# Kernel tuning notes

Measured on AMD Instinct MI355X. Metric: run time of the kernel, lower is better.

## Reference

```python
import jax, jax.numpy as jnp
import numpy as np
import math

B, L, E, H, G = 2, 128, 1024, 16, 8
D = E // H   # head_dim = 64
R = H // G   # query heads per kv head = 2


def setup_inputs() -> dict:
    key = jax.random.key(0)
    ks = jax.random.split(key, 12)
    def nrm(k, shape, s=1.0):
        return jax.random.normal(k, shape, dtype=jnp.float32) * s
    return {
        "Q": nrm(ks[0], (B, L, E)),
        "K": nrm(ks[1], (B, L, E)),
        "V": nrm(ks[2], (B, L, E)),
        "rpe": nrm(ks[3], (B, L, L, E)),
        "ln_g": jnp.ones((E,), jnp.float32),
        "ln_b": jnp.zeros((E,), jnp.float32),
        "Wq": nrm(ks[4], (E, H * D), 0.02), "bq": jnp.zeros((H * D,), jnp.float32),
        "Wk": nrm(ks[5], (E, G * D), 0.02), "bk": jnp.zeros((G * D,), jnp.float32),
        "Wv": nrm(ks[6], (E, G * D), 0.02), "bv": jnp.zeros((G * D,), jnp.float32),
        "Wrk": nrm(ks[7], (E, G * D), 0.02), "brk": jnp.zeros((G * D,), jnp.float32),
        "Wrv": nrm(ks[8], (E, G * D), 0.02), "brv": jnp.zeros((G * D,), jnp.float32),
        "Wo": nrm(ks[9], (E, E), 0.02), "bo": jnp.zeros((E,), jnp.float32),
    }


def _layernorm(x, g, b, eps=1e-5):
    mu = jnp.mean(x, axis=-1, keepdims=True)
    var = jnp.var(x, axis=-1, keepdims=True)
    return (x - mu) * jax.lax.rsqrt(var + eps) * g + b


def reference(Q, K, V, rpe, ln_g, ln_b, Wq, bq, Wk, bk, Wv, bv, Wrk, brk, Wrv, brv, Wo, bo):
    q = (Q @ Wq + bq).reshape(B, L, H, D).transpose(0, 2, 1, 3)   # [B,H,L,D]
    k = (K @ Wk + bk).reshape(B, L, G, D).transpose(0, 2, 1, 3)   # [B,G,L,D]
    v = (V @ Wv + bv).reshape(B, L, G, D).transpose(0, 2, 1, 3)   # [B,G,L,D]

    rn = _layernorm(rpe, ln_g, ln_b)                              # [B,L,L,E]
    rpe_k = (rn @ Wrk + brk).reshape(B, L, L, G, D).transpose(0, 3, 1, 2, 4)  # [B,G,L,L,D]
    rpe_v = (rn @ Wrv + brv).reshape(B, L, L, G, D).transpose(0, 3, 1, 2, 4)

    # Group query heads: head h = g*R + r maps to kv group g (repeat_interleave semantics).
    qg = q.reshape(B, G, R, L, D)
    # score[b,h,i,j] = q[b,h,i] . (k[b,g,i] + rpe_k[b,g,i,j]) / sqrt(D)
    # (note: the original pairs q_i with k_i, only rpe_k carries j-dependence)
    base = jnp.einsum('bgrid,bgid->bgri', qg, k)                  # j-independent q.k
    cross = jnp.einsum('bgrid,bgijd->bgrij', qg, rpe_k)
    scores = (base[..., None] + cross) / math.sqrt(D)             # [B,G,R,L,L]

    # Faithful to F.softmax over flattened L*L axis per head.
    attn = jax.nn.softmax(scores.reshape(B, G, R, L * L), axis=-1).reshape(B, G, R, L, L)

    # qv[b,h,i] = sum_j attn[b,h,i,j] * (v[b,g,i] + rpe_v[b,g,i,j])
    wsum = jnp.sum(attn, axis=-1)                                 # [B,G,R,L]
    qv = wsum[..., None] * v[:, :, None] + jnp.einsum('bgrij,bgijd->bgrid', attn, rpe_v)
    qv = qv.reshape(B, H, L, D).transpose(0, 2, 1, 3).reshape(B, L, E)
    return qv @ Wo + bo
```

## Files before the change

### kernel.cpp

```cpp
#include <hip/hip_runtime.h>


__global__ __launch_bounds__(256) void k_zero(
    const float* __restrict__ bq, const float* __restrict__ bk, const float* __restrict__ bv,
    const float* __restrict__ bo,
    float* __restrict__ q_ws, float* __restrict__ k_ws, float* __restrict__ v_ws,
    float* __restrict__ qv_ws, float* __restrict__ out, float* __restrict__ Gu_ws)
{
  int rr = blockIdx.x, tid = threadIdx.x;
#pragma unroll
  for (int s = 0; s < 4; s++) {
    int i = tid + s * 256;
    q_ws[rr * 1024 + i] = bq[i];
    qv_ws[rr * 1024 + i] = 0.f;
    out[rr * 1024 + i] = bo[i];
  }
#pragma unroll
  for (int s = 0; s < 2; s++) {
    int i = tid + s * 256;
    k_ws[rr * 512 + i] = bk[i];
    v_ws[rr * 512 + i] = bv[i];
  }
  int t = rr * 256 + tid;
  if (t < 4096) Gu_ws[t] = 0.f;
}

__global__ __launch_bounds__(256) void k_qkv(
    const float* __restrict__ Q, const float* __restrict__ K, const float* __restrict__ V,
    const float* __restrict__ Wq, const float* __restrict__ Wk, const float* __restrict__ Wv,
    float* __restrict__ q_ws, float* __restrict__ k_ws, float* __restrict__ v_ws)
{
  __shared__ float xs[8][256];
  int ct = blockIdx.x, rt = blockIdx.y, es = blockIdx.z, tid = threadIdx.x;
  const float* X; const float* W; float* out; int ldW, ldO, c0;
  if (ct < 4)      { X = Q; W = Wq; out = q_ws; ldW = 1024; ldO = 1024; c0 = ct * 256; }
  else if (ct < 6) { X = K; W = Wk; out = k_ws; ldW = 512;  ldO = 512;  c0 = (ct - 4) * 256; }
  else             { X = V; W = Wv; out = v_ws; ldW = 512;  ldO = 512;  c0 = (ct - 6) * 256; }
  int row0 = rt * 8, e0 = es * 256;
  for (int f = tid; f < 512; f += 256) {
    int r = f >> 6, e4 = f & 63;
    *(float4*)&xs[r][e4 * 4] = *(const float4*)(X + (size_t)(row0 + r) * 1024 + e0 + e4 * 4);
  }
  __syncthreads();
  int cg = tid & 63, rs = tid >> 6;
  int c = c0 + cg * 4;
  const float* wp = W + (size_t)e0 * ldW + c;
  float a0[4] = {0, 0, 0, 0}, a1[4] = {0, 0, 0, 0};
  float4 wc = *(const float4*)wp;
  for (int e = 0; e < 256; e++) {
    int en = e + 1 < 256 ? e + 1 : 255;
    float4 wn = *(const float4*)(wp + (size_t)en * ldW);
    float x0 = xs[rs][e], x1 = xs[rs + 4][e];
    a0[0] += x0 * wc.x; a0[1] += x0 * wc.y; a0[2] += x0 * wc.z; a0[3] += x0 * wc.w;
    a1[0] += x1 * wc.x; a1[1] += x1 * wc.y; a1[2] += x1 * wc.z; a1[3] += x1 * wc.w;
    wc = wn;
  }
#pragma unroll
  for (int s = 0; s < 4; s++) {
    atomicAdd(out + (size_t)(row0 + rs) * ldO + c + s, a0[s]);
    atomicAdd(out + (size_t)(row0 + rs + 4) * ldO + c + s, a1[s]);
  }
}

__global__ __launch_bounds__(256) void k_base(
    const float* __restrict__ q_ws, const float* __restrict__ k_ws,
    const float* __restrict__ brk, float* __restrict__ S0_ws)
{
  int t = blockIdx.x * 256 + threadIdx.x;
  int r = t >> 4, h = t & 15, g = h >> 1;
  const float* qp = q_ws + r * 1024 + h * 64;
  const float* kp = k_ws + r * 512 + g * 64;
  const float* bp = brk + g * 64;
  float s = 0.f;
#pragma unroll
  for (int d4 = 0; d4 < 16; d4++) {
    float4 q4 = *(const float4*)(qp + d4 * 4);
    float4 k4 = *(const float4*)(kp + d4 * 4);
    float4 b4 = *(const float4*)(bp + d4 * 4);
    s += q4.x * (k4.x + b4.x) + q4.y * (k4.y + b4.y)
       + q4.z * (k4.z + b4.z) + q4.w * (k4.w + b4.w);
  }
  S0_ws[t] = s * 0.125f;
}

__global__ __launch_bounds__(256) void k_uproj(
    const float* __restrict__ q_ws, const float* __restrict__ Wrk,
    const float* __restrict__ lng, const float* __restrict__ lnb,
    float* __restrict__ ut_ws, float* __restrict__ Gu_ws, float* __restrict__ S0_ws)
{
  __shared__ float wt[64][128];
  __shared__ float qs[32][64];
  int et = blockIdx.x, rrt = blockIdx.y, g = blockIdx.z, tid = threadIdx.x;
  int e0 = et * 128, rr0 = rrt * 16;
  for (int f = tid; f < 2048; f += 256) {
    int er = f >> 4, dq = f & 15;
    float4 p = *(const float4*)(Wrk + (size_t)(e0 + er) * 512 + g * 64 + dq * 4);
    wt[dq * 4 + 0][er] = p.x; wt[dq * 4 + 1][er] = p.y;
    wt[dq * 4 + 2][er] = p.z; wt[dq * 4 + 3][er] = p.w;
  }
  for (int f = tid; f < 512; f += 256) {
    int m = f >> 4, dq = f & 15;
    int rr = rr0 + (m >> 1), h = g * 2 + (m & 1);
    float4 p = *(const float4*)(q_ws + (size_t)rr * 1024 + h * 64 + dq * 4);
    qs[m][dq * 4 + 0] = p.x; qs[m][dq * 4 + 1] = p.y;
    qs[m][dq * 4 + 2] = p.z; qs[m][dq * 4 + 3] = p.w;
  }
  __syncthreads();
  int eg = tid & 31, rs = tid >> 5;
  float acc[4][4];
#pragma unroll
  for (int i = 0; i < 4; i++)
#pragma unroll
    for (int s = 0; s < 4; s++) acc[i][s] = 0.f;
  for (int d = 0; d < 64; d++) {
    float4 wv = *(float4*)&wt[d][eg * 4];
#pragma unroll
    for (int i = 0; i < 4; i++) {
      float qv = qs[rs * 4 + i][d];
      acc[i][0] += qv * wv.x; acc[i][1] += qv * wv.y;
      acc[i][2] += qv * wv.z; acc[i][3] += qv * wv.w;
    }
  }
#pragma unroll
  for (int k = 0; k < 2; k++) {
    int rr = rr0 + rs * 2 + k;
#pragma unroll
    for (int s = 0; s < 4; s++) {
      int e = e0 + eg * 4 + s;
      float2 st;
      st.x = acc[2 * k][s] * 0.125f;
      st.y = acc[2 * k + 1][s] * 0.125f;
      *(float2*)(ut_ws + ((size_t)rr * 1024 + e) * 16 + g * 2) = st;
    }
  }
  float4 ge4 = *(const float4*)(lng + e0 + eg * 4);
  float4 be4 = *(const float4*)(lnb + e0 + eg * 4);
#pragma unroll
  for (int i = 0; i < 4; i++) {
    float pg = 0.125f * (ge4.x * acc[i][0] + ge4.y * acc[i][1] + ge4.z * acc[i][2] + ge4.w * acc[i][3]);
    float pb = 0.125f * (be4.x * acc[i][0] + be4.y * acc[i][1] + be4.z * acc[i][2] + be4.w * acc[i][3]);
#pragma unroll
    for (int mk = 16; mk >= 1; mk >>= 1) { pg += __shfl_xor(pg, mk); pb += __shfl_xor(pb, mk); }
    if (eg == 0) {
      int m = rs * 4 + i;
      int rr = rr0 + (m >> 1), h = g * 2 + (m & 1);
      atomicAdd(Gu_ws + rr * 16 + h, pg);
      atomicAdd(S0_ws + rr * 16 + h, pb);
    }
  }
}

__global__ __launch_bounds__(128) void k_dotp(
    const float* __restrict__ rpe, const float* __restrict__ lng,
    const float* __restrict__ ut_ws, const float* __restrict__ Gu_ws,
    const float* __restrict__ S0_ws,
    float* __restrict__ s_ws, float* __restrict__ mu_ws, float* __restrict__ rs_ws)
{
  __shared__ float xs[32][68];
  __shared__ float us_t[16][68];
  int jt = blockIdx.x, rr = blockIdx.y, tid = threadIdx.x;
  int hq = tid & 7, jq = tid >> 3;
  int j0 = jt * 32;
  float acc[2][2] = {{0.f, 0.f}, {0.f, 0.f}};
  float sx[2] = {0.f, 0.f}, sq[2] = {0.f, 0.f};

  for (int ec = 0; ec < 16; ec++) {
    int eb = ec * 64;
    __syncthreads();
#pragma unroll
    for (int it = 0; it < 4; it++) {
      int f = it * 128 + tid;
      int row = f >> 4, e4 = f & 15;
      *(float4*)&xs[row][e4 * 4] =
          *(const float4*)(rpe + ((size_t)(rr * 128 + j0 + row)) * 1024 + eb + e4 * 4);
    }
#pragma unroll
    for (int it = 0; it < 2; it++) {
      int f = it * 128 + tid;
      int e = f >> 2, hh = f & 3;
      float4 u4 = *(const float4*)(ut_ws + ((size_t)rr * 1024 + eb + e) * 16 + hh * 4);
      float ge = lng[eb + e];
      us_t[hh * 4 + 0][e] = u4.x * ge;
      us_t[hh * 4 + 1][e] = u4.y * ge;
      us_t[hh * 4 + 2][e] = u4.z * ge;
      us_t[hh * 4 + 3][e] = u4.w * ge;
    }
    __syncthreads();
#pragma unroll
    for (int e4 = 0; e4 < 16; e4++) {
      float4 u0 = *(float4*)&us_t[hq * 2 + 0][e4 * 4];
      float4 u1 = *(float4*)&us_t[hq * 2 + 1][e4 * 4];
#pragma unroll
      for (int i = 0; i < 2; i++) {
        float4 xv = *(float4*)&xs[jq * 2 + i][e4 * 4];
        acc[i][0] += xv.x * u0.x + xv.y * u0.y + xv.z * u0.z + xv.w * u0.w;
        acc[i][1] += xv.x * u1.x + xv.y * u1.y + xv.z * u1.z + xv.w * u1.w;
        sx[i] += xv.x + xv.y + xv.z + xv.w;
        sq[i] += xv.x * xv.x + xv.y * xv.y + xv.z * xv.z + xv.w * xv.w;
      }
    }
  }
  float2 Gu2 = *(const float2*)(Gu_ws + rr * 16 + hq * 2);
  float2 S02 = *(const float2*)(S0_ws + rr * 16 + hq * 2);
#pragma unroll
  for (int i = 0; i < 2; i++) {
    int j = j0 + jq * 2 + i;
    float mu = sx[i] * (1.f / 1024.f);
    float rsv = rsqrtf(fmaxf(sq[i] * (1.f / 1024.f) - mu * mu, 0.f) + 1e-5f);
    float2 o;
    o.x = S02.x + rsv * (acc[i][0] - mu * Gu2.x);
    o.y = S02.y + rsv * (acc[i][1] - mu * Gu2.y);
    *(float2*)(s_ws + ((size_t)rr * 128 + j) * 16 + hq * 2) = o;
    if (hq == 0) { mu_ws[rr * 128 + j] = mu; rs_ws[rr * 128 + j] = rsv; }
  }
}

__global__ __launch_bounds__(256) void k_attn_p(
    const float* __restrict__ mu_ws, const float* __restrict__ rs_ws,
    float* __restrict__ s_ws,
    float* __restrict__ M_ws, float* __restrict__ Z_ws, float* __restrict__ C1_ws)
{
  int rr = blockIdx.x, tid = threadIdx.x;
  int h = tid >> 4, jl = tid & 15;
  float sv[8];
  float m = -1e30f;
#pragma unroll
  for (int k = 0; k < 8; k++) {
    int j = jl + k * 16;
    sv[k] = s_ws[((size_t)rr * 128 + j) * 16 + h];
    m = fmaxf(m, sv[k]);
  }
#pragma unroll
  for (int mk = 8; mk >= 1; mk >>= 1) m = fmaxf(m, __shfl_xor(m, mk, 16));
  float z = 0.f, c1 = 0.f;
#pragma unroll
  for (int k = 0; k < 8; k++) {
    int j = jl + k * 16;
    float p = expf(sv[k] - m);
    z += p;
    float p2 = p * rs_ws[rr * 128 + j];
    c1 += p2 * mu_ws[rr * 128 + j];
    s_ws[((size_t)rr * 128 + j) * 16 + h] = p2;
  }
#pragma unroll
  for (int mk = 8; mk >= 1; mk >>= 1) { z += __shfl_xor(z, mk, 16); c1 += __shfl_xor(c1, mk, 16); }
  if (jl == 0) {
    M_ws[rr * 16 + h] = m; Z_ws[rr * 16 + h] = z; C1_ws[rr * 16 + h] = c1;
  }
}

__global__ __launch_bounds__(128) void k_comb(
    const float* __restrict__ M_ws, const float* __restrict__ Z_ws, float* __restrict__ sc_ws)
{
  __shared__ float red[128];
  int b = blockIdx.x >> 4, h = blockIdx.x & 15;
  int i = threadIdx.x;
  int idx = ((b << 7) + i) * 16 + h;
  float ml = M_ws[idx];
  red[i] = ml;
  __syncthreads();
  for (int s = 64; s >= 1; s >>= 1) {
    if (i < s) red[i] = fmaxf(red[i], red[i + s]);
    __syncthreads();
  }
  float mg = red[0];
  __syncthreads();
  float zl = Z_ws[idx] * expf(ml - mg);
  red[i] = zl;
  __syncthreads();
  for (int s = 64; s >= 1; s >>= 1) {
    if (i < s) red[i] += red[i + s];
    __syncthreads();
  }
  float zg = red[0];
  sc_ws[idx] = expf(ml - mg) / zg;
}

__global__ __launch_bounds__(256) void k_wun(
    const float* __restrict__ rpe, const float* __restrict__ lng, const float* __restrict__ lnb,
    const float* __restrict__ p2_ws,
    const float* __restrict__ Z_ws, const float* __restrict__ C1_ws,
    float* __restrict__ w_ws)
{
  __shared__ float xs[16][512];
  __shared__ float p2s[128][16];
  __shared__ float C1S[16], ZS[16];
  int es = blockIdx.x, rr = blockIdx.y, tid = threadIdx.x;
  int e0 = es * 512;
#pragma unroll
  for (int it = 0; it < 2; it++) {
    int f = it * 256 + tid;
    int jj = f >> 2, hh = f & 3;
    *(float4*)&p2s[jj][hh * 4] = *(const float4*)(p2_ws + ((size_t)rr * 128 + jj) * 16 + hh * 4);
  }
  if (tid < 16) { C1S[tid] = C1_ws[rr * 16 + tid]; ZS[tid] = Z_ws[rr * 16 + tid]; }
  float acc[2][16];
#pragma unroll
  for (int i = 0; i < 2; i++)
#pragma unroll
    for (int h = 0; h < 16; h++) acc[i][h] = 0.f;

#define WUN_ROW(ii, xval) \
  acc[ii][0] += (xval) * p0.x;  acc[ii][1] += (xval) * p0.y;  \
  acc[ii][2] += (xval) * p0.z;  acc[ii][3] += (xval) * p0.w;  \
  acc[ii][4] += (xval) * p1.x;  acc[ii][5] += (xval) * p1.y;  \
  acc[ii][6] += (xval) * p1.z;  acc[ii][7] += (xval) * p1.w;  \
  acc[ii][8] += (xval) * p2v.x; acc[ii][9] += (xval) * p2v.y; \
  acc[ii][10] += (xval) * p2v.z; acc[ii][11] += (xval) * p2v.w; \
  acc[ii][12] += (xval) * p3.x; acc[ii][13] += (xval) * p3.y; \
  acc[ii][14] += (xval) * p3.z; acc[ii][15] += (xval) * p3.w;

  for (int jc = 0; jc < 8; jc++) {
    __syncthreads();
#pragma unroll
    for (int it = 0; it < 8; it++) {
      int f = it * 256 + tid;
      int row = f >> 7, e4 = f & 127;
      *(float4*)&xs[row][e4 * 4] =
          *(const float4*)(rpe + ((size_t)(rr * 128 + jc * 16 + row)) * 1024 + e0 + e4 * 4);
    }
    __syncthreads();
#pragma unroll
    for (int j = 0; j < 16; j++) {
      int jj = jc * 16 + j;
      float2 xv = *(float2*)&xs[j][tid * 2];
      float4 p0 = *(float4*)&p2s[jj][0];
      float4 p1 = *(float4*)&p2s[jj][4];
      float4 p2v = *(float4*)&p2s[jj][8];
      float4 p3 = *(float4*)&p2s[jj][12];
      WUN_ROW(0, xv.x)
      WUN_ROW(1, xv.y)
    }
  }
#undef WUN_ROW

#pragma unroll
  for (int i = 0; i < 2; i++) {
    int e = e0 + tid * 2 + i;
    float ge = lng[e], be = lnb[e];
    float* wp = w_ws + ((size_t)rr * 1024 + e) * 16;
#pragma unroll
    for (int hh = 0; hh < 4; hh++) {
      float4 o;
      o.x = ge * (acc[i][hh * 4 + 0] - C1S[hh * 4 + 0]) + be * ZS[hh * 4 + 0];
      o.y = ge * (acc[i][hh * 4 + 1] - C1S[hh * 4 + 1]) + be * ZS[hh * 4 + 1];
      o.z = ge * (acc[i][hh * 4 + 2] - C1S[hh * 4 + 2]) + be * ZS[hh * 4 + 2];
      o.w = ge * (acc[i][hh * 4 + 3] - C1S[hh * 4 + 3]) + be * ZS[hh * 4 + 3];
      *(float4*)(wp + hh * 4) = o;
    }
  }
}

__global__ __launch_bounds__(256) void k_qv(
    const float* __restrict__ w_ws, const float* __restrict__ Wrv,
    float* __restrict__ qv_ws)
{
  __shared__ float As[32][133];
  int g = blockIdx.x, rrt = blockIdx.y, es = blockIdx.z, tid = threadIdx.x;
  int rr0 = rrt * 16, e0 = es * 128;
  for (int f = tid; f < 2048; f += 256) {
    int rl = f >> 7, e = f & 127;
    float2 w2 = *(const float2*)(w_ws + ((size_t)(rr0 + rl) * 1024 + e0 + e) * 16 + g * 2);
    As[rl * 2 + 0][e] = w2.x;
    As[rl * 2 + 1][e] = w2.y;
  }
  __syncthreads();
  int cl = tid & 15, ms = tid >> 4;
  const float* wp = Wrv + (size_t)e0 * 512 + g * 64 + cl * 4;
  float acc[2][4];
#pragma unroll
  for (int hh = 0; hh < 2; hh++)
#pragma unroll
    for (int s = 0; s < 4; s++) acc[hh][s] = 0.f;
  float4 wc = *(const float4*)wp;
  for (int e = 0; e < 128; e++) {
    int en = e + 1 < 128 ? e + 1 : 127;
    float4 wn = *(const float4*)(wp + (size_t)en * 512);
    float a0 = As[ms * 2][e], a1 = As[ms * 2 + 1][e];
    acc[0][0] += a0 * wc.x; acc[0][1] += a0 * wc.y; acc[0][2] += a0 * wc.z; acc[0][3] += a0 * wc.w;
    acc[1][0] += a1 * wc.x; acc[1][1] += a1 * wc.y; acc[1][2] += a1 * wc.z; acc[1][3] += a1 * wc.w;
    wc = wn;
  }
  int rr = rr0 + ms;
#pragma unroll
  for (int hh = 0; hh < 2; hh++) {
    float* qp = qv_ws + (size_t)rr * 1024 + (g * 2 + hh) * 64 + cl * 4;
#pragma unroll
    for (int s = 0; s < 4; s++) atomicAdd(qp + s, acc[hh][s]);
  }
}

__global__ __launch_bounds__(256) void k_out(
    const float* __restrict__ qv_ws, const float* __restrict__ v_ws,
    const float* __restrict__ brv, const float* __restrict__ Z_ws,
    const float* __restrict__ sc_ws, const float* __restrict__ Wo,
    float* __restrict__ out)
{
  __shared__ float xs[8][128];
  int ct = blockIdx.x, rt = blockIdx.y, es = blockIdx.z, tid = threadIdx.x;
  int row0 = rt * 8, e0 = es * 128, c0 = ct * 256;
  for (int f = tid; f < 1024; f += 256) {
    int r = f >> 7, ei = f & 127;
    int e = e0 + ei, row = row0 + r;
    int h = e >> 6, gg = h >> 1, dl = e & 63;
    float vb = v_ws[row * 512 + gg * 64 + dl] + brv[gg * 64 + dl];
    xs[r][ei] = sc_ws[row * 16 + h] * (Z_ws[row * 16 + h] * vb + qv_ws[(size_t)row * 1024 + e]);
  }
  __syncthreads();
  int cg = tid & 63, rs = tid >> 6;
  int c = c0 + cg * 4;
  const float* wp = Wo + (size_t)e0 * 1024 + c;
  float a0[4] = {0, 0, 0, 0}, a1[4] = {0, 0, 0, 0};
  float4 wc = *(const float4*)wp;
  for (int e = 0; e < 128; e++) {
    int en = e + 1 < 128 ? e + 1 : 127;
    float4 wn = *(const float4*)(wp + (size_t)en * 1024);
    float x0 = xs[rs][e], x1 = xs[rs + 4][e];
    a0[0] += x0 * wc.x; a0[1] += x0 * wc.y; a0[2] += x0 * wc.z; a0[3] += x0 * wc.w;
    a1[0] += x1 * wc.x; a1[1] += x1 * wc.y; a1[2] += x1 * wc.z; a1[3] += x1 * wc.w;
    wc = wn;
  }
#pragma unroll
  for (int s = 0; s < 4; s++) {
    atomicAdd(out + (size_t)(row0 + rs) * 1024 + c + s, a0[s]);
    atomicAdd(out + (size_t)(row0 + rs + 4) * 1024 + c + s, a1[s]);
  }
}

extern "C" void kernel_launch(void* const* d_in, const int* in_sizes, int n_in,
                              void* d_out, int out_size, void* d_ws, size_t ws_size,
                              hipStream_t stream) {
  (void)in_sizes; (void)n_in; (void)out_size; (void)ws_size;
  const float* Q   = (const float*)d_in[0];
  const float* K   = (const float*)d_in[1];
  const float* V   = (const float*)d_in[2];
  const float* rpe = (const float*)d_in[3];
  const float* lng = (const float*)d_in[4];
  const float* lnb = (const float*)d_in[5];
  const float* Wq  = (const float*)d_in[6];
  const float* bq  = (const float*)d_in[7];
  const float* Wk  = (const float*)d_in[8];
  const float* bk  = (const float*)d_in[9];
  const float* Wv  = (const float*)d_in[10];
  const float* bv  = (const float*)d_in[11];
  const float* Wrk = (const float*)d_in[12];
  const float* brk = (const float*)d_in[13];
  const float* Wrv = (const float*)d_in[14];
  const float* brv = (const float*)d_in[15];
  const float* Wo  = (const float*)d_in[16];
  const float* bo  = (const float*)d_in[17];
  float* out = (float*)d_out;

  float* ws    = (float*)d_ws;
  float* q_ws  = ws;
  float* k_ws  = q_ws + 262144;
  float* v_ws  = k_ws + 131072;
  float* ut_ws = v_ws + 131072;
  float* S0_ws = ut_ws + 4194304;
  float* Gu_ws = S0_ws + 4096;
  float* s_ws  = Gu_ws + 4096;
  float* mu_ws = s_ws + 524288;
  float* rs_ws = mu_ws + 32768;
  float* M_ws  = rs_ws + 32768;
  float* Z_ws  = M_ws + 4096;
  float* C1_ws = Z_ws + 4096;
  float* sc_ws = C1_ws + 4096;
  float* qv_ws = sc_ws + 4096;
  float* w_ws  = ut_ws;

  k_zero<<<256, 256, 0, stream>>>(bq, bk, bv, bo, q_ws, k_ws, v_ws, qv_ws, out, Gu_ws);
  k_qkv<<<dim3(8, 32, 4), 256, 0, stream>>>(Q, K, V, Wq, Wk, Wv, q_ws, k_ws, v_ws);
  k_base<<<16, 256, 0, stream>>>(q_ws, k_ws, brk, S0_ws);
  k_uproj<<<dim3(8, 16, 8), 256, 0, stream>>>(q_ws, Wrk, lng, lnb, ut_ws, Gu_ws, S0_ws);
  k_dotp<<<dim3(4, 256), 128, 0, stream>>>(rpe, lng, ut_ws, Gu_ws, S0_ws, s_ws, mu_ws, rs_ws);
  k_attn_p<<<256, 256, 0, stream>>>(mu_ws, rs_ws, s_ws, M_ws, Z_ws, C1_ws);
  k_comb<<<32, 128, 0, stream>>>(M_ws, Z_ws, sc_ws);
  k_wun<<<dim3(2, 256), 256, 0, stream>>>(rpe, lng, lnb, s_ws, Z_ws, C1_ws, w_ws);
  k_qv<<<dim3(8, 16, 8), 256, 0, stream>>>(w_ws, Wrv, qv_ws);
  k_out<<<dim3(4, 32, 8), 256, 0, stream>>>(qv_ws, v_ws, brv, Z_ws, sc_ws, Wo, out);
}
```

Measured before the change: 506.8 us.

## Split k_dotp reduction over E into two halves and finalize in k_attn_p

The rpe dot-product kernel now splits the 1024-wide embedding reduction into two halves across a new grid dimension, doubling block count. Partial dot products and partial sum/sumsq statistics go to separate buffers, and the layernorm normalization and score assembly move into k_attn_p, which adds the two partials. Each thread now computes only part of the row sum/sumsq (a redundancy removal), followed by a shuffle reduction. This adds extra workspace traffic and requires the workspace to be large enough for the new buffers.

```diff
diff --git a/kernel.cpp b/kernel.cpp
--- a/kernel.cpp
+++ b/kernel.cpp
@@ -152,20 +152,22 @@
 
 __global__ __launch_bounds__(128) void k_dotp(
     const float* __restrict__ rpe, const float* __restrict__ lng,
-    const float* __restrict__ ut_ws, const float* __restrict__ Gu_ws,
-    const float* __restrict__ S0_ws,
-    float* __restrict__ s_ws, float* __restrict__ mu_ws, float* __restrict__ rs_ws)
+    const float* __restrict__ ut_ws,
+    float* __restrict__ sraw0, float* __restrict__ sraw1,
+    float* __restrict__ sxp0, float* __restrict__ sxp1,
+    float* __restrict__ sqp0, float* __restrict__ sqp1)
 {
   __shared__ float xs[32][68];
   __shared__ float us_t[16][68];
-  int jt = blockIdx.x, rr = blockIdx.y, tid = threadIdx.x;
+  int jt = blockIdx.x, rr = blockIdx.y, et = blockIdx.z, tid = threadIdx.x;
   int hq = tid & 7, jq = tid >> 3;
   int j0 = jt * 32;
+  int ebase = et * 512;
   float acc[2][2] = {{0.f, 0.f}, {0.f, 0.f}};
   float sx[2] = {0.f, 0.f}, sq[2] = {0.f, 0.f};
 
-  for (int ec = 0; ec < 16; ec++) {
-    int eb = ec * 64;
+  for (int ec = 0; ec < 8; ec++) {
+    int eb = ebase + ec * 64;
     __syncthreads();
 #pragma unroll
     for (int it = 0; it < 4; it++) {
@@ -195,39 +197,64 @@
         float4 xv = *(float4*)&xs[jq * 2 + i][e4 * 4];
         acc[i][0] += xv.x * u0.x + xv.y * u0.y + xv.z * u0.z + xv.w * u0.w;
         acc[i][1] += xv.x * u1.x + xv.y * u1.y + xv.z * u1.z + xv.w * u1.w;
+      }
+    }
+#pragma unroll
+    for (int t = 0; t < 2; t++) {
+      int e4s = t * 8 + hq;
+#pragma unroll
+      for (int i = 0; i < 2; i++) {
+        float4 xv = *(float4*)&xs[jq * 2 + i][e4s * 4];
         sx[i] += xv.x + xv.y + xv.z + xv.w;
         sq[i] += xv.x * xv.x + xv.y * xv.y + xv.z * xv.z + xv.w * xv.w;
       }
     }
   }
-  float2 Gu2 = *(const float2*)(Gu_ws + rr * 16 + hq * 2);
-  float2 S02 = *(const float2*)(S0_ws + rr * 16 + hq * 2);
+  float* sr = (et == 0) ? sraw0 : sraw1;
+  float* sxp = (et == 0) ? sxp0 : sxp1;
+  float* sqp = (et == 0) ? sqp0 : sqp1;
 #pragma unroll
   for (int i = 0; i < 2; i++) {
     int j = j0 + jq * 2 + i;
-    float mu = sx[i] * (1.f / 1024.f);
-    float rsv = rsqrtf(fmaxf(sq[i] * (1.f / 1024.f) - mu * mu, 0.f) + 1e-5f);
-    float2 o;
-    o.x = S02.x + rsv * (acc[i][0] - mu * Gu2.x);
-    o.y = S02.y + rsv * (acc[i][1] - mu * Gu2.y);
-    *(float2*)(s_ws + ((size_t)rr * 128 + j) * 16 + hq * 2) = o;
-    if (hq == 0) { mu_ws[rr * 128 + j] = mu; rs_ws[rr * 128 + j] = rsv; }
+    float2 o; o.x = acc[i][0]; o.y = acc[i][1];
+    *(float2*)(sr + ((size_t)rr * 128 + j) * 16 + hq * 2) = o;
+#pragma unroll
+    for (int mk = 4; mk >= 1; mk >>= 1) {
+      sx[i] += __shfl_xor(sx[i], mk, 8);
+      sq[i] += __shfl_xor(sq[i], mk, 8);
+    }
+    if (hq == 0) {
+      sxp[rr * 128 + j] = sx[i];
+      sqp[rr * 128 + j] = sq[i];
+    }
   }
 }
 
 __global__ __launch_bounds__(256) void k_attn_p(
-    const float* __restrict__ mu_ws, const float* __restrict__ rs_ws,
+    const float* __restrict__ sraw0, const float* __restrict__ sraw1,
+    const float* __restrict__ sxp0, const float* __restrict__ sxp1,
+    const float* __restrict__ sqp0, const float* __restrict__ sqp1,
+    const float* __restrict__ Gu_ws, const float* __restrict__ S0_ws,
     float* __restrict__ s_ws,
     float* __restrict__ M_ws, float* __restrict__ Z_ws, float* __restrict__ C1_ws)
 {
   int rr = blockIdx.x, tid = threadIdx.x;
   int h = tid >> 4, jl = tid & 15;
-  float sv[8];
+  float Gv = Gu_ws[rr * 16 + h];
+  float S0v = S0_ws[rr * 16 + h];
+  float sv[8], muv[8], rsvv[8];
   float m = -1e30f;
 #pragma unroll
   for (int k = 0; k < 8; k++) {
     int j = jl + k * 16;
-    sv[k] = s_ws[((size_t)rr * 128 + j) * 16 + h];
+    size_t idx = ((size_t)rr * 128 + j) * 16 + h;
+    float sxv = sxp0[rr * 128 + j] + sxp1[rr * 128 + j];
+    float sqv = sqp0[rr * 128 + j] + sqp1[rr * 128 + j];
+    float mu = sxv * (1.f / 1024.f);
+    float rsv = rsqrtf(fmaxf(sqv * (1.f / 1024.f) - mu * mu, 0.f) + 1e-5f);
+    float accv = sraw0[idx] + sraw1[idx];
+    sv[k] = S0v + rsv * (accv - mu * Gv);
+    muv[k] = mu; rsvv[k] = rsv;
     m = fmaxf(m, sv[k]);
   }
 #pragma unroll
@@ -238,8 +265,8 @@
     int j = jl + k * 16;
     float p = expf(sv[k] - m);
     z += p;
-    float p2 = p * rs_ws[rr * 128 + j];
-    c1 += p2 * mu_ws[rr * 128 + j];
+    float p2 = p * rsvv[k];
+    c1 += p2 * muv[k];
     s_ws[((size_t)rr * 128 + j) * 16 + h] = p2;
   }
 #pragma unroll
@@ -466,14 +493,22 @@
   float* C1_ws = Z_ws + 4096;
   float* sc_ws = C1_ws + 4096;
   float* qv_ws = sc_ws + 4096;
+  float* sraw0 = qv_ws + 262144;
+  float* sraw1 = sraw0 + 524288;
+  float* sxp0  = sraw1 + 524288;
+  float* sxp1  = sxp0 + 32768;
+  float* sqp0  = sxp1 + 32768;
+  float* sqp1  = sqp0 + 32768;
   float* w_ws  = ut_ws;
 
   k_zero<<<256, 256, 0, stream>>>(bq, bk, bv, bo, q_ws, k_ws, v_ws, qv_ws, out, Gu_ws);
   k_qkv<<<dim3(8, 32, 4), 256, 0, stream>>>(Q, K, V, Wq, Wk, Wv, q_ws, k_ws, v_ws);
   k_base<<<16, 256, 0, stream>>>(q_ws, k_ws, brk, S0_ws);
   k_uproj<<<dim3(8, 16, 8), 256, 0, stream>>>(q_ws, Wrk, lng, lnb, ut_ws, Gu_ws, S0_ws);
-  k_dotp<<<dim3(4, 256), 128, 0, stream>>>(rpe, lng, ut_ws, Gu_ws, S0_ws, s_ws, mu_ws, rs_ws);
-  k_attn_p<<<256, 256, 0, stream>>>(mu_ws, rs_ws, s_ws, M_ws, Z_ws, C1_ws);
+  k_dotp<<<dim3(4, 256, 2), 128, 0, stream>>>(rpe, lng, ut_ws,
+                                              sraw0, sraw1, sxp0, sxp1, sqp0, sqp1);
+  k_attn_p<<<256, 256, 0, stream>>>(sraw0, sraw1, sxp0, sxp1, sqp0, sqp1,
+                                    Gu_ws, S0_ws, s_ws, M_ws, Z_ws, C1_ws);
   k_comb<<<32, 128, 0, stream>>>(M_ws, Z_ws, sc_ws);
   k_wun<<<dim3(2, 256), 256, 0, stream>>>(rpe, lng, lnb, s_ws, Z_ws, C1_ws, w_ws);
   k_qv<<<dim3(8, 16, 8), 256, 0, stream>>>(w_ws, Wrv, qv_ws);
```

After: 470.7 us. -7.1%, faster.
